# Performance work log

Measured on AMD Instinct MI355X. Metric: run time of the kernel, lower is better.

The kernel has to match this reference:

```python
import jax, jax.numpy as jnp
import numpy as np

EPS = 1e-8  # torch nn.CosineSimilarity default eps


def setup_inputs() -> dict:
    key = jax.random.key(0)
    k1, k2 = jax.random.split(key)
    query = jax.random.normal(k1, (8, 2048, 64), dtype=jnp.float32)
    y = jax.random.normal(k2, (8, 2048, 64), dtype=jnp.float32)
    return {"query": query, "y": y}


def _l2_normalize(x):
    # x / max(||x||, eps) along last dim (matches torch cosine_similarity clamping)
    n = jnp.sqrt(jnp.sum(x * x, axis=-1, keepdims=True))
    return x / jnp.maximum(n, EPS)


def reference(query, y):
    # Algebraically equivalent to broadcast CosineSimilarity over [B,Lq,Ly,D]:
    # normalize once, then batched GEMM -> [B, Lq, Ly]
    qn = _l2_normalize(query)          # [B, Lq, D]
    yn = _l2_normalize(y)              # [B, Ly, D]
    att = jnp.einsum("bqd,bkd->bqk", qn, yn)  # [B, Lq, Ly]
    sim = jnp.max(att, axis=2)[:, None, :]     # [B, 1, Lq]
    return (att, sim)
```

## Files before the change

### kernel.cpp

```cpp
#include <hip/hip_runtime.h>

#define LL 2048
#define DD 64
#define BB 8
#define EPSF 1e-8f

#define NELEM ((size_t)BB * LL * DD)

typedef short bf16x8 __attribute__((ext_vector_type(8)));
typedef float f32x4 __attribute__((ext_vector_type(4)));

__device__ __forceinline__ ushort f2bf(float f) {
    uint u = __float_as_uint(f);
    return (ushort)((u + 0x7fffu + ((u >> 16) & 1u)) >> 16);
}
__device__ __forceinline__ float bf2f(ushort h) {
    return __uint_as_float((uint)h << 16);
}

__global__ __launch_bounds__(256) void norm_split_kernel(
    const float* __restrict__ q, const float* __restrict__ y,
    ushort* __restrict__ ws) {
    const int row   = blockIdx.x * 32 + (threadIdx.x >> 3);
    const int oct   = threadIdx.x & 7;
    const int which = blockIdx.y;
    const float* src = which ? y : q;
    ushort* hi = ws + (size_t)which * NELEM;
    ushort* lo = ws + 2 * NELEM + (size_t)which * NELEM;

    const float* g = src + (size_t)row * DD;
    float4 v0 = *reinterpret_cast<const float4*>(g + oct * 4);
    float4 v1 = *reinterpret_cast<const float4*>(g + 32 + oct * 4);
    float ss = v0.x*v0.x + v0.y*v0.y + v0.z*v0.z + v0.w*v0.w
             + v1.x*v1.x + v1.y*v1.y + v1.z*v1.z + v1.w*v1.w;
    ss += __shfl_xor(ss, 1);
    ss += __shfl_xor(ss, 2);
    ss += __shfl_xor(ss, 4);
    const float sc = 1.0f / fmaxf(sqrtf(ss), EPSF);

    const float f[8] = {v0.x*sc, v0.y*sc, v0.z*sc, v0.w*sc,
                        v1.x*sc, v1.y*sc, v1.z*sc, v1.w*sc};
    ushort h[8], l8[8];
    #pragma unroll
    for (int i = 0; i < 8; ++i) {
        h[i]  = f2bf(f[i]);
        l8[i] = f2bf(f[i] - bf2f(h[i]));
    }
    const size_t base = (size_t)row * DD + oct * 4;
    *reinterpret_cast<ushort4*>(hi + base)      = make_ushort4(h[0], h[1], h[2], h[3]);
    *reinterpret_cast<ushort4*>(hi + base + 32) = make_ushort4(h[4], h[5], h[6], h[7]);
    *reinterpret_cast<ushort4*>(lo + base)      = make_ushort4(l8[0], l8[1], l8[2], l8[3]);
    *reinterpret_cast<ushort4*>(lo + base + 32) = make_ushort4(l8[4], l8[5], l8[6], l8[7]);
}

__global__ __launch_bounds__(256) void att_mfma_kernel(
    const ushort* __restrict__ ws, float* __restrict__ out) {
    const int b       = blockIdx.y;
    const int rowBase = blockIdx.x * 32;
    const int t  = threadIdx.x;
    const int w  = t >> 6;
    const int l  = t & 63;
    const int ln = l & 15;
    const int kg = l >> 4;

    const ushort* qh = ws;
    const ushort* yh = ws + NELEM;
    const ushort* ql = ws + 2 * NELEM;
    const ushort* yl = ws + 3 * NELEM;

    bf16x8 ah[2][2], alo[2][2];
    #pragma unroll
    for (int m = 0; m < 2; ++m)
        #pragma unroll
        for (int kk = 0; kk < 2; ++kk) {
            const size_t off =
                ((size_t)(b * LL + rowBase + m * 16 + ln)) * DD + kk * 32 + kg * 8;
            ah[m][kk]  = *reinterpret_cast<const bf16x8*>(qh + off);
            alo[m][kk] = *reinterpret_cast<const bf16x8*>(ql + off);
        }

    float rmax[2][4];
    #pragma unroll
    for (int m = 0; m < 2; ++m)
        #pragma unroll
        for (int j = 0; j < 4; ++j) rmax[m][j] = -1e30f;

    for (int ct = 0; ct < 8; ++ct) {
        const int colBase = ct * 256 + w * 64;

        bf16x8 bh[4][2], bl[4][2];
        #pragma unroll
        for (int n = 0; n < 4; ++n)
            #pragma unroll
            for (int kk = 0; kk < 2; ++kk) {
                const size_t off =
                    ((size_t)(b * LL + colBase + n * 16 + ln)) * DD + kk * 32 + kg * 8;
                bh[n][kk] = *reinterpret_cast<const bf16x8*>(yh + off);
                bl[n][kk] = *reinterpret_cast<const bf16x8*>(yl + off);
            }

        f32x4 acc[2][4];
        #pragma unroll
        for (int m = 0; m < 2; ++m)
            #pragma unroll
            for (int n = 0; n < 4; ++n)
                acc[m][n] = (f32x4){0.f, 0.f, 0.f, 0.f};

        #pragma unroll
        for (int kk = 0; kk < 2; ++kk)
            #pragma unroll
            for (int m = 0; m < 2; ++m)
                #pragma unroll
                for (int n = 0; n < 4; ++n)
                    acc[m][n] = __builtin_amdgcn_mfma_f32_16x16x32_bf16(
                        alo[m][kk], bh[n][kk], acc[m][n], 0, 0, 0);
        #pragma unroll
        for (int kk = 0; kk < 2; ++kk)
            #pragma unroll
            for (int m = 0; m < 2; ++m)
                #pragma unroll
                for (int n = 0; n < 4; ++n)
                    acc[m][n] = __builtin_amdgcn_mfma_f32_16x16x32_bf16(
                        ah[m][kk], bl[n][kk], acc[m][n], 0, 0, 0);
        #pragma unroll
        for (int kk = 0; kk < 2; ++kk)
            #pragma unroll
            for (int m = 0; m < 2; ++m)
                #pragma unroll
                for (int n = 0; n < 4; ++n)
                    acc[m][n] = __builtin_amdgcn_mfma_f32_16x16x32_bf16(
                        ah[m][kk], bh[n][kk], acc[m][n], 0, 0, 0);

        float* po = out + ((size_t)(b * LL + rowBase)) * LL + colBase;
        #pragma unroll
        for (int m = 0; m < 2; ++m)
            #pragma unroll
            for (int n = 0; n < 4; ++n)
                #pragma unroll
                for (int j = 0; j < 4; ++j) {
                    const float v = acc[m][n][j];
                    po[(size_t)(m * 16 + kg * 4 + j) * LL + n * 16 + ln] = v;
                    rmax[m][j] = fmaxf(rmax[m][j], v);
                }
    }

    #pragma unroll
    for (int m = 0; m < 2; ++m)
        #pragma unroll
        for (int j = 0; j < 4; ++j) {
            float v = rmax[m][j];
            v = fmaxf(v, __shfl_xor(v, 1));
            v = fmaxf(v, __shfl_xor(v, 2));
            v = fmaxf(v, __shfl_xor(v, 4));
            v = fmaxf(v, __shfl_xor(v, 8));
            rmax[m][j] = v;
        }

    __shared__ float smax[4][32];
    if (ln == 0) {
        #pragma unroll
        for (int m = 0; m < 2; ++m)
            #pragma unroll
            for (int j = 0; j < 4; ++j)
                smax[w][m * 16 + kg * 4 + j] = rmax[m][j];
    }
    __syncthreads();
    if (t < 32) {
        const float v = fmaxf(fmaxf(smax[0][t], smax[1][t]),
                              fmaxf(smax[2][t], smax[3][t]));
        out[(size_t)BB * LL * LL + (size_t)b * LL + rowBase + t] = v;
    }
}

extern "C" void kernel_launch(void* const* d_in, const int* in_sizes, int n_in,
                              void* d_out, int out_size, void* d_ws, size_t ws_size,
                              hipStream_t stream) {
    const float* q = (const float*)d_in[0];
    const float* y = (const float*)d_in[1];
    float* out     = (float*)d_out;
    ushort* ws     = (ushort*)d_ws;

    norm_split_kernel<<<dim3(512, 2), dim3(256), 0, stream>>>(q, y, ws);
    att_mfma_kernel<<<dim3(LL / 32, BB), dim3(256), 0, stream>>>(ws, out);
}
```

Baseline: 161.6 us.

## Transpose MFMA operands for vectorized stores and double-buffer Y fragment loads

Swaps the MFMA operand order so each lane holds four consecutive columns of one output row, which allows a single 16-byte vector store per fragment instead of four scattered scalar stores. The Y hi/lo fragments are double-buffered across column tiles so the next tile's global loads are issued while the current tile is being computed and stored. The row-max reduction is reworked to fit the new layout, and launch bounds request two blocks per SIMD. The extra register buffers raise register pressure, and the occupancy hint may force spills.

```diff
diff --git a/kernel.cpp b/kernel.cpp
--- a/kernel.cpp
+++ b/kernel.cpp
@@ -53,7 +53,7 @@
     *reinterpret_cast<ushort4*>(lo + base + 32) = make_ushort4(l8[4], l8[5], l8[6], l8[7]);
 }
 
-__global__ __launch_bounds__(256) void att_mfma_kernel(
+__global__ __launch_bounds__(256, 2) void att_mfma_kernel(
     const ushort* __restrict__ ws, float* __restrict__ out) {
     const int b       = blockIdx.y;
     const int rowBase = blockIdx.x * 32;
@@ -68,101 +68,100 @@
     const ushort* ql = ws + 2 * NELEM;
     const ushort* yl = ws + 3 * NELEM;
 
-    bf16x8 ah[2][2], alo[2][2];
+    bf16x8 qhf[2][2], qlf[2][2];
     #pragma unroll
-    for (int m = 0; m < 2; ++m)
+    for (int mq = 0; mq < 2; ++mq)
         #pragma unroll
         for (int kk = 0; kk < 2; ++kk) {
             const size_t off =
-                ((size_t)(b * LL + rowBase + m * 16 + ln)) * DD + kk * 32 + kg * 8;
-            ah[m][kk]  = *reinterpret_cast<const bf16x8*>(qh + off);
-            alo[m][kk] = *reinterpret_cast<const bf16x8*>(ql + off);
+                ((size_t)(b * LL + rowBase + mq * 16 + ln)) * DD + kk * 32 + kg * 8;
+            qhf[mq][kk] = *reinterpret_cast<const bf16x8*>(qh + off);
+            qlf[mq][kk] = *reinterpret_cast<const bf16x8*>(ql + off);
         }
 
-    float rmax[2][4];
+    float rmax[2] = {-1e30f, -1e30f};
+
+    bf16x8 yh0[4][2], yl0[4][2], yh1[4][2], yl1[4][2];
+
+#define LOADY(DH, DL, CT) do {                                                   \
+    const int colBase_ = (CT) * 256 + w * 64;                                    \
+    _Pragma("unroll")                                                            \
+    for (int ny = 0; ny < 4; ++ny) {                                             \
+        _Pragma("unroll")                                                        \
+        for (int kk = 0; kk < 2; ++kk) {                                         \
+            const size_t off_ =                                                  \
+                ((size_t)(b * LL + colBase_ + ny * 16 + ln)) * DD + kk * 32 + kg * 8; \
+            DH[ny][kk] = *reinterpret_cast<const bf16x8*>(yh + off_);            \
+            DL[ny][kk] = *reinterpret_cast<const bf16x8*>(yl + off_);            \
+        }                                                                        \
+    }                                                                            \
+} while (0)
+
+#define COMPSTORE(SH, SL, CT) do {                                               \
+    const int colBase_ = (CT) * 256 + w * 64;                                    \
+    f32x4 acc[2][4];                                                             \
+    _Pragma("unroll")                                                            \
+    for (int mq = 0; mq < 2; ++mq)                                               \
+        _Pragma("unroll")                                                        \
+        for (int ny = 0; ny < 4; ++ny)                                           \
+            acc[mq][ny] = (f32x4){0.f, 0.f, 0.f, 0.f};                           \
+    _Pragma("unroll")                                                            \
+    for (int kk = 0; kk < 2; ++kk)                                               \
+        _Pragma("unroll")                                                        \
+        for (int mq = 0; mq < 2; ++mq)                                           \
+            _Pragma("unroll")                                                    \
+            for (int ny = 0; ny < 4; ++ny)                                       \
+                acc[mq][ny] = __builtin_amdgcn_mfma_f32_16x16x32_bf16(           \
+                    SL[ny][kk], qhf[mq][kk], acc[mq][ny], 0, 0, 0);              \
+    _Pragma("unroll")                                                            \
+    for (int kk = 0; kk < 2; ++kk)                                               \
+        _Pragma("unroll")                                                        \
+        for (int mq = 0; mq < 2; ++mq)                                           \
+            _Pragma("unroll")                                                    \
+            for (int ny = 0; ny < 4; ++ny)                                       \
+                acc[mq][ny] = __builtin_amdgcn_mfma_f32_16x16x32_bf16(           \
+                    SH[ny][kk], qlf[mq][kk], acc[mq][ny], 0, 0, 0);              \
+    _Pragma("unroll")                                                            \
+    for (int kk = 0; kk < 2; ++kk)                                               \
+        _Pragma("unroll")                                                        \
+        for (int mq = 0; mq < 2; ++mq)                                           \
+            _Pragma("unroll")                                                    \
+            for (int ny = 0; ny < 4; ++ny)                                       \
+                acc[mq][ny] = __builtin_amdgcn_mfma_f32_16x16x32_bf16(           \
+                    SH[ny][kk], qhf[mq][kk], acc[mq][ny], 0, 0, 0);              \
+    _Pragma("unroll")                                                            \
+    for (int mq = 0; mq < 2; ++mq) {                                             \
+        _Pragma("unroll")                                                        \
+        for (int ny = 0; ny < 4; ++ny) {                                         \
+            f32x4 v = acc[mq][ny];                                               \
+            *reinterpret_cast<f32x4*>(                                           \
+                out + ((size_t)(b * LL + rowBase + mq * 16 + ln)) * LL           \
+                    + colBase_ + ny * 16 + kg * 4) = v;                          \
+            rmax[mq] = fmaxf(rmax[mq],                                           \
+                       fmaxf(fmaxf(v[0], v[1]), fmaxf(v[2], v[3])));             \
+        }                                                                        \
+    }                                                                            \
+} while (0)
+
+    LOADY(yh0, yl0, 0);
     #pragma unroll
-    for (int m = 0; m < 2; ++m)
-        #pragma unroll
-        for (int j = 0; j < 4; ++j) rmax[m][j] = -1e30f;
-
-    for (int ct = 0; ct < 8; ++ct) {
-        const int colBase = ct * 256 + w * 64;
-
-        bf16x8 bh[4][2], bl[4][2];
-        #pragma unroll
-        for (int n = 0; n < 4; ++n)
-            #pragma unroll
-            for (int kk = 0; kk < 2; ++kk) {
-                const size_t off =
-                    ((size_t)(b * LL + colBase + n * 16 + ln)) * DD + kk * 32 + kg * 8;
-                bh[n][kk] = *reinterpret_cast<const bf16x8*>(yh + off);
-                bl[n][kk] = *reinterpret_cast<const bf16x8*>(yl + off);
-            }
-
-        f32x4 acc[2][4];
-        #pragma unroll
-        for (int m = 0; m < 2; ++m)
-            #pragma unroll
-            for (int n = 0; n < 4; ++n)
-                acc[m][n] = (f32x4){0.f, 0.f, 0.f, 0.f};
-
-        #pragma unroll
-        for (int kk = 0; kk < 2; ++kk)
-            #pragma unroll
-            for (int m = 0; m < 2; ++m)
-                #pragma unroll
-                for (int n = 0; n < 4; ++n)
-                    acc[m][n] = __builtin_amdgcn_mfma_f32_16x16x32_bf16(
-                        alo[m][kk], bh[n][kk], acc[m][n], 0, 0, 0);
-        #pragma unroll
-        for (int kk = 0; kk < 2; ++kk)
-            #pragma unroll
-            for (int m = 0; m < 2; ++m)
-                #pragma unroll
-                for (int n = 0; n < 4; ++n)
-                    acc[m][n] = __builtin_amdgcn_mfma_f32_16x16x32_bf16(
-                        ah[m][kk], bl[n][kk], acc[m][n], 0, 0, 0);
-        #pragma unroll
-        for (int kk = 0; kk < 2; ++kk)
-            #pragma unroll
-            for (int m = 0; m < 2; ++m)
-                #pragma unroll
-                for (int n = 0; n < 4; ++n)
-                    acc[m][n] = __builtin_amdgcn_mfma_f32_16x16x32_bf16(
-                        ah[m][kk], bh[n][kk], acc[m][n], 0, 0, 0);
-
-        float* po = out + ((size_t)(b * LL + rowBase)) * LL + colBase;
-        #pragma unroll
-        for (int m = 0; m < 2; ++m)
-            #pragma unroll
-            for (int n = 0; n < 4; ++n)
-                #pragma unroll
-                for (int j = 0; j < 4; ++j) {
-                    const float v = acc[m][n][j];
-                    po[(size_t)(m * 16 + kg * 4 + j) * LL + n * 16 + ln] = v;
-                    rmax[m][j] = fmaxf(rmax[m][j], v);
-                }
+    for (int ct = 0; ct < 8; ct += 2) {
+        if (ct + 1 < 8) LOADY(yh1, yl1, ct + 1);
+        COMPSTORE(yh0, yl0, ct);
+        if (ct + 2 < 8) LOADY(yh0, yl0, ct + 2);
+        if (ct + 1 < 8) COMPSTORE(yh1, yl1, ct + 1);
     }
 
     #pragma unroll
-    for (int m = 0; m < 2; ++m)
-        #pragma unroll
-        for (int j = 0; j < 4; ++j) {
-            float v = rmax[m][j];
-            v = fmaxf(v, __shfl_xor(v, 1));
-            v = fmaxf(v, __shfl_xor(v, 2));
-            v = fmaxf(v, __shfl_xor(v, 4));
-            v = fmaxf(v, __shfl_xor(v, 8));
-            rmax[m][j] = v;
-        }
+    for (int mq = 0; mq < 2; ++mq) {
+        rmax[mq] = fmaxf(rmax[mq], __shfl_xor(rmax[mq], 16));
+        rmax[mq] = fmaxf(rmax[mq], __shfl_xor(rmax[mq], 32));
+    }
 
     __shared__ float smax[4][32];
-    if (ln == 0) {
-        #pragma unroll
-        for (int m = 0; m < 2; ++m)
-            #pragma unroll
-            for (int j = 0; j < 4; ++j)
-                smax[w][m * 16 + kg * 4 + j] = rmax[m][j];
+    if (kg == 0) {
+        smax[w][ln]      = rmax[0];
+        smax[w][16 + ln] = rmax[1];
     }
     __syncthreads();
     if (t < 32) {
@@ -170,6 +169,8 @@
                               fmaxf(smax[2][t], smax[3][t]));
         out[(size_t)BB * LL * LL + (size_t)b * LL + rowBase + t] = v;
     }
+#undef LOADY
+#undef COMPSTORE
 }
 
 extern "C" void kernel_launch(void* const* d_in, const int* in_sizes, int n_in,
```

Measured after the change: 164.4 us. About the same (+1.7%).
